# Performance work log

Hardware: AMD Instinct MI355X
Metric: run time of the kernel (lower is better)

The kernel has to match this reference:

```python
import jax, jax.numpy as jnp
import numpy as np

EPS = 1e-8  # torch CosineSimilarity default eps


def setup_inputs() -> dict:
    key = jax.random.key(0)
    k1, k2, k3, k4, k5, k6, k7, k8 = jax.random.split(key, 8)
    N1, N2 = 8192, 8192
    # first 3 cols: geometric features; col 3: integer class label stored as float
    e1_feat = jax.random.normal(k1, (N1, 3), dtype=jnp.float32)
    e2_feat = jax.random.normal(k2, (N2, 3), dtype=jnp.float32)
    e1_cls = jax.random.randint(k3, (N1, 1), 0, 8).astype(jnp.float32)
    e2_cls = jax.random.randint(k4, (N2, 1), 0, 8).astype(jnp.float32)
    edges1 = jnp.concatenate([e1_feat, e1_cls], axis=-1)
    edges2 = jnp.concatenate([e2_feat, e2_cls], axis=-1)
    W1 = jax.random.normal(k5, (3, 64), dtype=jnp.float32) * 0.5
    b1 = jax.random.normal(k6, (64,), dtype=jnp.float32) * 0.1
    W2 = jax.random.normal(k7, (64, 32), dtype=jnp.float32) * 0.1
    b2 = jax.random.normal(k8, (32,), dtype=jnp.float32) * 0.1
    return {"edges1": edges1, "edges2": edges2, "W1": W1, "b1": b1, "W2": W2, "b2": b2}


def _branch(x, W1, b1, W2, b2):
    h = jax.nn.relu(x @ W1 + b1)
    return h @ W2 + b2  # [N, 32]


def reference(edges1, edges2, W1, b1, W2, b2):
    f1 = _branch(edges1[:, :3], W1, b1, W2, b2)  # [N1, 32]
    f2 = _branch(edges2[:, :3], W1, b1, W2, b2)  # [N2, 32]
    # pairwise cosine similarity without materializing [N1, N2, 32]
    dots = jnp.einsum('id,jd->ij', f1, f2)                  # [N1, N2]
    n1 = jnp.linalg.norm(f1, axis=-1)                        # [N1]
    n2 = jnp.linalg.norm(f2, axis=-1)                        # [N2]
    denom = jnp.maximum(n1[:, None] * n2[None, :], EPS)
    dist_mat = dots / denom                                  # [N1, N2]
    # pairwise label-equality mask (all label columns must match)
    cls1 = edges1[:, 3:].astype(jnp.int32)                   # [N1, C]
    cls2 = edges2[:, 3:].astype(jnp.int32)                   # [N2, C]
    cls_aff = jnp.all(cls1[:, None, :] == cls2[None, :, :], axis=-1)  # [N1, N2] bool
    return cls_aff.astype(dist_mat.dtype) * dist_mat
```

## Files before the change

### kernel.cpp

```cpp
#include <hip/hip_runtime.h>


typedef __bf16 bf16x8 __attribute__((ext_vector_type(8)));
typedef float floatx4 __attribute__((ext_vector_type(4)));

__global__ __launch_bounds__(256) void mlp_norm_kernel(
    const float* __restrict__ e1, const float* __restrict__ e2,
    const float* __restrict__ W1, const float* __restrict__ b1,
    const float* __restrict__ W2, const float* __restrict__ b2,
    __bf16* __restrict__ f1b, __bf16* __restrict__ f2b,
    int* __restrict__ cls1, int* __restrict__ cls2, int N1, int N2)
{
    __shared__ float sW1[192];
    __shared__ float sb1[64];
    __shared__ float sW2[2048];
    __shared__ float sb2[32];
    for (int i = threadIdx.x; i < 192; i += 256) sW1[i] = W1[i];
    if (threadIdx.x < 64) sb1[threadIdx.x] = b1[threadIdx.x];
    for (int i = threadIdx.x; i < 2048; i += 256) sW2[i] = W2[i];
    if (threadIdx.x < 32) sb2[threadIdx.x] = b2[threadIdx.x];
    __syncthreads();

    int t = blockIdx.x * 256 + threadIdx.x;
    if (t >= N1 + N2) return;

    const float* src;
    __bf16* fout;
    int* cout;
    int row;
    if (t < N1) { row = t;      src = e1 + (size_t)row * 4; fout = f1b; cout = cls1; }
    else        { row = t - N1; src = e2 + (size_t)row * 4; fout = f2b; cout = cls2; }

    float x0 = src[0], x1 = src[1], x2 = src[2];
    int lbl = (int)src[3];

    float f[32];
#pragma unroll
    for (int k = 0; k < 32; ++k) f[k] = sb2[k];

    for (int j = 0; j < 64; ++j) {
        float h = fmaf(x0, sW1[j], fmaf(x1, sW1[64 + j], fmaf(x2, sW1[128 + j], sb1[j])));
        h = fmaxf(h, 0.0f);
#pragma unroll
        for (int k = 0; k < 32; ++k) f[k] = fmaf(h, sW2[j * 32 + k], f[k]);
    }

    float ss = 0.0f;
#pragma unroll
    for (int k = 0; k < 32; ++k) ss = fmaf(f[k], f[k], ss);
    float n = sqrtf(ss);
    float scale = (n > 1e-20f) ? (1.0f / n) : 0.0f;

    __bf16* dst = fout + (size_t)row * 32;
#pragma unroll
    for (int k = 0; k < 32; ++k) dst[k] = (__bf16)(f[k] * scale);
    cout[row] = lbl;
}

__global__ __launch_bounds__(256) void pair_cos_kernel(
    const __bf16* __restrict__ f1b, const __bf16* __restrict__ f2b,
    const int* __restrict__ cls1, const int* __restrict__ cls2,
    float* __restrict__ out, int N2, int ncg)
{
    const int lane = threadIdx.x & 63;
    const int wid = blockIdx.x * 4 + (threadIdx.x >> 6);
    const int istrip = wid / ncg;
    const int cg = wid - istrip * ncg;
    const int i0 = istrip * 16;
    const int j0 = cg * 512;
    const int r16 = lane & 15;
    const int q = lane >> 4;

    bf16x8 a = *(const bf16x8*)(f1b + (size_t)(i0 + r16) * 32 + q * 8);
    int4 c1 = *(const int4*)(cls1 + i0 + q * 4);

    const size_t row_base = (size_t)(i0 + q * 4) * N2;

#pragma unroll 4
    for (int tIdx = 0; tIdx < 32; ++tIdx) {
        int j = j0 + tIdx * 16;
        bf16x8 b = *(const bf16x8*)(f2b + (size_t)(j + r16) * 32 + q * 8);
        int c2 = cls2[j + r16];

        floatx4 acc = {0.0f, 0.0f, 0.0f, 0.0f};
        floatx4 d = __builtin_amdgcn_mfma_f32_16x16x32_bf16(a, b, acc, 0, 0, 0);

        float* outp = out + row_base + j + r16;
        outp[0]            = (c1.x == c2) ? d[0] : 0.0f;
        outp[(size_t)N2]   = (c1.y == c2) ? d[1] : 0.0f;
        outp[(size_t)N2*2] = (c1.z == c2) ? d[2] : 0.0f;
        outp[(size_t)N2*3] = (c1.w == c2) ? d[3] : 0.0f;
    }
}

extern "C" void kernel_launch(void* const* d_in, const int* in_sizes, int n_in,
                              void* d_out, int out_size, void* d_ws, size_t ws_size,
                              hipStream_t stream) {
    const float* e1 = (const float*)d_in[0];
    const float* e2 = (const float*)d_in[1];
    const float* W1 = (const float*)d_in[2];
    const float* b1 = (const float*)d_in[3];
    const float* W2 = (const float*)d_in[4];
    const float* b2 = (const float*)d_in[5];
    float* out = (float*)d_out;

    const int N1 = in_sizes[0] / 4;
    const int N2 = in_sizes[1] / 4;

    char* ws = (char*)d_ws;
    __bf16* f1b = (__bf16*)ws;
    __bf16* f2b = (__bf16*)(ws + (size_t)N1 * 64);
    int* cls1 = (int*)(ws + (size_t)(N1 + N2) * 64);
    int* cls2 = cls1 + N1;

    int nrows = N1 + N2;
    mlp_norm_kernel<<<(nrows + 255) / 256, 256, 0, stream>>>(
        e1, e2, W1, b1, W2, b2, f1b, f2b, cls1, cls2, N1, N2);

    int ncg = N2 / 512;
    int nwaves = (N1 / 16) * ncg;
    pair_cos_kernel<<<nwaves / 4, 256, 0, stream>>>(
        f1b, f2b, cls1, cls2, out, N2, ncg);
}
```

Before: 277.6 us.

## Stage MFMA outputs through LDS for coalesced vector nontemporal stores

The pair kernel now writes each wave's 16x64 masked tile into a per-wave LDS buffer and reads it back transposed, so each lane emits 16-byte nontemporal stores along contiguous rows in place of scattered 4-byte stores. Four MFMAs are issued per batch before the epilogue. The MLP kernel is also relaunched with 64-thread blocks to spread it across more CUs. The transposition relies on wave-local lockstep with lgkmcnt waits and no barrier, and it adds LDS traffic.

New measurement: 290.9 us. 4.8% more time.

```diff
diff --git a/kernel.cpp b/kernel.cpp
--- a/kernel.cpp
+++ b/kernel.cpp
@@ -4,7 +4,7 @@
 typedef __bf16 bf16x8 __attribute__((ext_vector_type(8)));
 typedef float floatx4 __attribute__((ext_vector_type(4)));
 
-__global__ __launch_bounds__(256) void mlp_norm_kernel(
+__global__ __launch_bounds__(64) void mlp_norm_kernel(
     const float* __restrict__ e1, const float* __restrict__ e2,
     const float* __restrict__ W1, const float* __restrict__ b1,
     const float* __restrict__ W2, const float* __restrict__ b2,
@@ -15,13 +15,13 @@
     __shared__ float sb1[64];
     __shared__ float sW2[2048];
     __shared__ float sb2[32];
-    for (int i = threadIdx.x; i < 192; i += 256) sW1[i] = W1[i];
+    for (int i = threadIdx.x; i < 192; i += 64) sW1[i] = W1[i];
     if (threadIdx.x < 64) sb1[threadIdx.x] = b1[threadIdx.x];
-    for (int i = threadIdx.x; i < 2048; i += 256) sW2[i] = W2[i];
+    for (int i = threadIdx.x; i < 2048; i += 64) sW2[i] = W2[i];
     if (threadIdx.x < 32) sb2[threadIdx.x] = b2[threadIdx.x];
     __syncthreads();
 
-    int t = blockIdx.x * 256 + threadIdx.x;
+    int t = blockIdx.x * 64 + threadIdx.x;
     if (t >= N1 + N2) return;
 
     const float* src;
@@ -62,8 +62,13 @@
     const int* __restrict__ cls1, const int* __restrict__ cls2,
     float* __restrict__ out, int N2, int ncg)
 {
-    const int lane = threadIdx.x & 63;
-    const int wid = blockIdx.x * 4 + (threadIdx.x >> 6);
+    __shared__ float lds[4][16 * 68];
+    const int tid = threadIdx.x;
+    const int lane = tid & 63;
+    const int w = tid >> 6;
+    float* wbuf = lds[w];
+
+    const int wid = blockIdx.x * 4 + w;
     const int istrip = wid / ncg;
     const int cg = wid - istrip * ncg;
     const int i0 = istrip * 16;
@@ -72,24 +77,37 @@
     const int q = lane >> 4;
 
     bf16x8 a = *(const bf16x8*)(f1b + (size_t)(i0 + r16) * 32 + q * 8);
-    int4 c1 = *(const int4*)(cls1 + i0 + q * 4);
+    int4 c1v = *(const int4*)(cls1 + i0 + q * 4);
+    int cc[4] = {c1v.x, c1v.y, c1v.z, c1v.w};
 
-    const size_t row_base = (size_t)(i0 + q * 4) * N2;
-
-#pragma unroll 4
-    for (int tIdx = 0; tIdx < 32; ++tIdx) {
-        int j = j0 + tIdx * 16;
-        bf16x8 b = *(const bf16x8*)(f2b + (size_t)(j + r16) * 32 + q * 8);
-        int c2 = cls2[j + r16];
-
-        floatx4 acc = {0.0f, 0.0f, 0.0f, 0.0f};
-        floatx4 d = __builtin_amdgcn_mfma_f32_16x16x32_bf16(a, b, acc, 0, 0, 0);
-
-        float* outp = out + row_base + j + r16;
-        outp[0]            = (c1.x == c2) ? d[0] : 0.0f;
-        outp[(size_t)N2]   = (c1.y == c2) ? d[1] : 0.0f;
-        outp[(size_t)N2*2] = (c1.z == c2) ? d[2] : 0.0f;
-        outp[(size_t)N2*3] = (c1.w == c2) ? d[3] : 0.0f;
+    for (int r = 0; r < 8; ++r) {
+        int jb = j0 + r * 64;
+        floatx4 d[4];
+        int c2[4];
+#pragma unroll
+        for (int t = 0; t < 4; ++t) {
+            int j = jb + t * 16;
+            bf16x8 b = *(const bf16x8*)(f2b + (size_t)(j + r16) * 32 + q * 8);
+            c2[t] = cls2[j + r16];
+            floatx4 z = {0.0f, 0.0f, 0.0f, 0.0f};
+            d[t] = __builtin_amdgcn_mfma_f32_16x16x32_bf16(a, b, z, 0, 0, 0);
+        }
+#pragma unroll
+        for (int t = 0; t < 4; ++t) {
+#pragma unroll
+            for (int m = 0; m < 4; ++m) {
+                float v = (cc[m] == c2[t]) ? d[t][m] : 0.0f;
+                wbuf[(q * 4 + m) * 68 + t * 16 + r16] = v;
+            }
+        }
+        asm volatile("s_waitcnt lgkmcnt(0)" ::: "memory");
+#pragma unroll
+        for (int k = 0; k < 4; ++k) {
+            floatx4 v = *(const floatx4*)(wbuf + (4 * k + q) * 68 + r16 * 4);
+            float* dst = out + (size_t)(i0 + 4 * k + q) * N2 + jb + r16 * 4;
+            __builtin_nontemporal_store(v, (floatx4*)dst);
+        }
+        asm volatile("s_waitcnt lgkmcnt(0)" ::: "memory");
     }
 }
 
@@ -114,7 +132,7 @@
     int* cls2 = cls1 + N1;
 
     int nrows = N1 + N2;
-    mlp_norm_kernel<<<(nrows + 255) / 256, 256, 0, stream>>>(
+    mlp_norm_kernel<<<(nrows + 63) / 64, 64, 0, stream>>>(
         e1, e2, W1, b1, W2, b2, f1b, f2b, cls1, cls2, N1, N2);
 
     int ncg = N2 / 512;
```
